# Performance work log

Hardware: AMD Instinct MI355X
Metric: run time of the kernel (lower is better)

## Reference

```python
import math
import jax, jax.numpy as jnp
import numpy as np

B, T, T_P, C, H = 4, 2048, 256, 768, 12
HD = C // H


def setup_inputs() -> dict:
    key = jax.random.key(0)
    k1, k2, k3, k4 = jax.random.split(key, 4)
    x = jax.random.normal(k1, (B, T, C), dtype=jnp.float32)
    prefix = jax.random.normal(k2, (B, T_P, C), dtype=jnp.float32)
    # torch nn.Linear weight layout: (out_features, in_features)
    W_qkv = jax.random.normal(k3, (3 * C, C), dtype=jnp.float32) * (1.0 / math.sqrt(C))
    W_out = jax.random.normal(k4, (C, C), dtype=jnp.float32) * (1.0 / math.sqrt(C))
    return {"x": x, "prefix": prefix, "W_qkv": W_qkv, "W_out": W_out}


def _mac_causal_mask(t_p: int, t: int) -> jnp.ndarray:
    total = t_p + t
    mask = jnp.zeros((total, total), dtype=bool)
    mask = mask.at[:t_p, t_p:].set(True)  # h tokens blocked from x tokens
    causal = jnp.triu(jnp.ones((t, t), dtype=bool), k=1)  # causal within x block
    return mask.at[t_p:, t_p:].set(causal)


def reference(x, prefix, W_qkv, W_out):
    b, t, c = x.shape
    t_p = prefix.shape[1]
    t_all = t_p + t
    x_full = jnp.concatenate([prefix, x], axis=1)          # (B, T_all, C)
    qkv = x_full @ W_qkv.T                                  # (B, T_all, 3C)
    q, k, v = jnp.split(qkv, 3, axis=-1)
    # (B, H, T_all, HD)
    q = q.reshape(b, t_all, H, HD).transpose(0, 2, 1, 3)
    k = k.reshape(b, t_all, H, HD).transpose(0, 2, 1, 3)
    v = v.reshape(b, t_all, H, HD).transpose(0, 2, 1, 3)
    scale = 1.0 / math.sqrt(HD)
    att = jnp.einsum('bhqd,bhkd->bhqk', q, k) * scale       # (B, H, T_all, T_all)
    mask = _mac_causal_mask(t_p, t)
    att = jnp.where(mask[None, None], -jnp.inf, att)
    att = jax.nn.softmax(att, axis=-1)                      # dropout = identity (eval)
    out = jnp.einsum('bhqk,bhkd->bhqd', att, v)             # (B, H, T_all, HD)
    out = out.transpose(0, 2, 1, 3).reshape(b, t_all, c)
    out = out @ W_out.T
    return out[:, t_p:, :]                                  # only x portion (B, T, C)
```

## Files before the change

### kernel.cpp

```cpp
#include <hip/hip_runtime.h>

constexpr int Bn   = 4;
constexpr int Tn   = 2048;
constexpr int TPn  = 256;
constexpr int TALLn = 2304;
constexpr int Cn   = 768;
constexpr int Hn   = 12;
constexpr int HDn  = 64;

typedef __bf16 bf16x4 __attribute__((ext_vector_type(4)));
typedef __bf16 bf16x8 __attribute__((ext_vector_type(8)));
typedef float  f32x4  __attribute__((ext_vector_type(4)));
typedef unsigned u32x4 __attribute__((ext_vector_type(4)));

__device__ __forceinline__ unsigned short f2bf(float f) {
    unsigned int x = __float_as_uint(f);
    x += 0x7fffu + ((x >> 16) & 1u);
    return (unsigned short)(x >> 16);
}

__device__ __forceinline__ unsigned cvt_pk_bf16(float a, float b) {
    unsigned r;
    asm("v_cvt_pk_bf16_f32 %0, %1, %2" : "=v"(r) : "v"(a), "v"(b));
    return r;
}

#define ASYNC16(gsrc, ldst)                                                           \
    __builtin_amdgcn_global_load_lds((__attribute__((address_space(1))) void*)(gsrc), \
                                     (__attribute__((address_space(3))) void*)(ldst), \
                                     16, 0, 0)

__global__ __launch_bounds__(256) void k_build_xfull(
        const float* __restrict__ x, const float* __restrict__ pre,
        unsigned short* __restrict__ xf) {
    int idx = blockIdx.x * 256 + threadIdx.x;
    int row = idx / (Cn / 4);
    int c   = (idx - row * (Cn / 4)) * 4;
    int b = row / TALLn, tt = row - b * TALLn;
    const float* src = (tt < TPn) ? pre + ((size_t)b * TPn + tt) * Cn + c
                                  : x   + ((size_t)b * Tn + (tt - TPn)) * Cn + c;
    float4 f = *reinterpret_cast<const float4*>(src);
    ushort4 o = { f2bf(f.x), f2bf(f.y), f2bf(f.z), f2bf(f.w) };
    *reinterpret_cast<ushort4*>(xf + (size_t)row * Cn + c) = o;
}

__global__ __launch_bounds__(256) void k_cast2(
        const float* __restrict__ wqkv, const float* __restrict__ wout,
        unsigned short* __restrict__ wqb, unsigned short* __restrict__ wob) {
    int idx = (blockIdx.x * 256 + threadIdx.x) * 4;
    const int n1 = 3 * Cn * Cn;
    const float* src;
    unsigned short* dst;
    if (idx < n1) { src = wqkv + idx; dst = wqb + idx; }
    else          { src = wout + (idx - n1); dst = wob + (idx - n1); }
    float4 f = *reinterpret_cast<const float4*>(src);
    ushort4 o = { f2bf(f.x), f2bf(f.y), f2bf(f.z), f2bf(f.w) };
    *reinterpret_cast<ushort4*>(dst) = o;
}

__global__ __launch_bounds__(256) void k_qkv_gemm(
        const unsigned short* __restrict__ A, const unsigned short* __restrict__ W,
        unsigned short* __restrict__ Qb, unsigned short* __restrict__ Kb,
        unsigned short* __restrict__ Vt) {
    __shared__ __align__(16) unsigned short smem[16384];
    const int tid  = threadIdx.x;
    const int wave = tid >> 6;
    const int lane = tid & 63;
    const int g = lane >> 4, l16 = lane & 15;
    const int m0 = blockIdx.x * 128, n0 = blockIdx.y * 128;
    const int wr = wave >> 1, wc = wave & 1;

    const unsigned short* pa[2];
    const unsigned short* pb[2];
    int sd[2];
    #pragma unroll
    for (int inst = 0; inst < 2; ++inst) {
        const int li = inst * 256 + tid;
        const int row = li >> 2;
        const int ch = (li & 3) ^ ((row >> 1) & 3);
        pa[inst] = A + (size_t)(m0 + row) * Cn + ch * 8;
        pb[inst] = W + (size_t)(n0 + row) * Cn + ch * 8;
        sd[inst] = (inst * 256 + wave * 64) * 8;
    }
    int aoff[4], boff[4];
    #pragma unroll
    for (int mt = 0; mt < 4; ++mt) {
        const int ra = wr * 64 + mt * 16 + l16;
        aoff[mt] = ra * 32 + ((g ^ ((ra >> 1) & 3)) << 3);
        const int rb = wc * 64 + mt * 16 + l16;
        boff[mt] = rb * 32 + ((g ^ ((rb >> 1) & 3)) << 3);
    }

    f32x4 acc[4][4] = {};

    #pragma unroll
    for (int inst = 0; inst < 2; ++inst) {
        ASYNC16(pa[inst], &smem[0]    + sd[inst]);
        ASYNC16(pb[inst], &smem[8192] + sd[inst]);
        pa[inst] += 32;
        pb[inst] += 32;
    }
    __syncthreads();

    int buf = 0;
    for (int kk = 0; kk < 24; ++kk) {
        if (kk + 1 < 24) {
            #pragma unroll
            for (int inst = 0; inst < 2; ++inst) {
                ASYNC16(pa[inst], &smem[(buf ^ 1) * 4096]        + sd[inst]);
                ASYNC16(pb[inst], &smem[8192 + (buf ^ 1) * 4096] + sd[inst]);
                pa[inst] += 32;
                pb[inst] += 32;
            }
        }
        const unsigned short* Ab = &smem[buf * 4096];
        const unsigned short* Bb = &smem[8192 + buf * 4096];
        bf16x8 af[4], bfv[4];
        #pragma unroll
        for (int mt = 0; mt < 4; ++mt) {
            af[mt]  = *reinterpret_cast<const bf16x8*>(&Ab[aoff[mt]]);
            bfv[mt] = *reinterpret_cast<const bf16x8*>(&Bb[boff[mt]]);
        }
        __builtin_amdgcn_s_setprio(1);
        #pragma unroll
        for (int mt = 0; mt < 4; ++mt)
            #pragma unroll
            for (int nt = 0; nt < 4; ++nt)
                acc[mt][nt] = __builtin_amdgcn_mfma_f32_16x16x32_bf16(
                        af[mt], bfv[nt], acc[mt][nt], 0, 0, 0);
        __builtin_amdgcn_s_setprio(0);
        buf ^= 1;
        __syncthreads();
    }

    const int b   = m0 / TALLn;
    const int t0  = m0 - b * TALLn;
    const int sel = n0 / Cn;
    const int hn0 = n0 - sel * Cn;
    constexpr float SCQ = 0.18033688011112042f;

    if (sel == 2) {
        #pragma unroll
        for (int mt = 0; mt < 4; ++mt)
            #pragma unroll
            for (int nt = 0; nt < 4; ++nt)
                #pragma unroll
                for (int r = 0; r < 4; ++r) {
                    const int t  = wr * 64 + mt * 16 + g * 4 + r;
                    const int hn = wc * 64 + nt * 16 + l16;
                    smem[hn * 128 + (((t >> 3) ^ (hn & 7)) << 3) + (t & 7)] =
                            f2bf(acc[mt][nt][r]);
                }
        __syncthreads();
        #pragma unroll
        for (int j = 0; j < 8; ++j) {
            const int u  = tid + 256 * j;
            const int hn = u >> 4, tc = u & 15;
            const int tile64 = tc >> 3;
            const int np = tc & 7;
            const int kg = np >> 2, gs = np & 3;
            const int tgA = tile64 * 8 + kg * 4 + (gs >> 1);
            const int sub = (gs & 1) * 4;
            bf16x4 rA = *reinterpret_cast<const bf16x4*>(
                    &smem[hn * 128 + ((tgA ^ (hn & 7)) << 3) + sub]);
            bf16x4 rB = *reinterpret_cast<const bf16x4*>(
                    &smem[hn * 128 + (((tgA + 2) ^ (hn & 7)) << 3) + sub]);
            bf16x8 v = __builtin_shufflevector(rA, rB, 0, 1, 2, 3, 4, 5, 6, 7);
            const int hh = (hn0 + hn) >> 6;
            const int dd = hn & 63;
            *reinterpret_cast<bf16x8*>(
                    &Vt[(((size_t)b * Hn + hh) * HDn + dd) * TALLn + t0 + tc * 8]) = v;
        }
    } else {
        #pragma unroll
        for (int mt = 0; mt < 4; ++mt)
            #pragma unroll
            for (int nt = 0; nt < 4; ++nt)
                #pragma unroll
                for (int r = 0; r < 4; ++r) {
                    const int t  = t0 + wr * 64 + mt * 16 + g * 4 + r;
                    const int hn = hn0 + wc * 64 + nt * 16 + l16;
                    const int h = hn >> 6, d = hn & 63;
                    if (sel == 0)
                        Qb[(((size_t)b * Hn + h) * TALLn + t) * HDn + d] =
                                f2bf(acc[mt][nt][r] * SCQ);
                    else
                        Kb[(((size_t)b * Hn + h) * TALLn + t) * HDn + d] =
                                f2bf(acc[mt][nt][r]);
                }
    }
}

__global__ __launch_bounds__(256) void k_attn(
        const unsigned short* __restrict__ Qb, const unsigned short* __restrict__ Kb,
        const unsigned short* __restrict__ Vt, unsigned short* __restrict__ Ob) {
    __shared__ __align__(16) unsigned short Ks[2][4096];
    __shared__ __align__(16) unsigned short Vs[2][4096];
    const int tid  = threadIdx.x;
    const int wq   = tid >> 6;
    const int lane = tid & 63;
    const int l16  = lane & 15;
    const int g    = lane >> 4;

    const int fb  = blockIdx.x;
    const int j   = fb >> 3;
    const int bh  = 6 * (fb & 7) + (j % 6);
    const int chunk = 31 - (j / 6);
    const int nkt = 5 + chunk;
    const size_t kv = (size_t)bh * TALLn * HDn;

    int koff[4][2];
    #pragma unroll
    for (int band = 0; band < 4; ++band)
        #pragma unroll
        for (int ks = 0; ks < 2; ++ks)
            koff[band][ks] = (band * 16 + l16) * 64 + (((ks * 4 + g) ^ (l16 & 7)) << 3);
    int voff[2];
    #pragma unroll
    for (int kg = 0; kg < 2; ++kg)
        voff[kg] = l16 * 64 + (((kg * 4 + g) ^ (l16 & 7)) << 3);
    const unsigned short* pk[2];
    const unsigned short* pv[2];
    int sdst[2];
    #pragma unroll
    for (int inst = 0; inst < 2; ++inst) {
        const int li = inst * 256 + tid;
        const int row = li >> 3;
        const int ch = (li & 7) ^ (row & 7);
        pk[inst] = Kb + kv + row * HDn + ch * 8;
        pv[inst] = Vt + kv + row * TALLn + ch * 8;
        sdst[inst] = (inst * 256 + wq * 64) * 8;
    }
    constexpr int KSTRIDE = 64 * HDn;
    constexpr int VSTRIDE = 64;

    bf16x8 qf[2];
    {
        const int tq = TPn + chunk * 64 + wq * 16 + l16;
        #pragma unroll
        for (int ks = 0; ks < 2; ++ks)
            qf[ks] = *reinterpret_cast<const bf16x8*>(
                    Qb + kv + (size_t)tq * HDn + ks * 32 + g * 8);
    }

    bf16x8 ones;
    #pragma unroll
    for (int i = 0; i < 8; ++i) ones[i] = (__bf16)1.0f;

    f32x4 oacc[4] = {};
    f32x4 lacc = {};

    #pragma unroll
    for (int inst = 0; inst < 2; ++inst) {
        ASYNC16(pk[inst], &Ks[0][0] + sdst[inst]);
        ASYNC16(pv[inst], &Vs[0][0] + sdst[inst]);
        pk[inst] += KSTRIDE;
        pv[inst] += VSTRIDE;
    }
    __syncthreads();

    int buf = 0;
    for (int t = 0; t < nkt; ++t) {
        if (t + 1 < nkt) {
            #pragma unroll
            for (int inst = 0; inst < 2; ++inst) {
                ASYNC16(pk[inst], &Ks[buf ^ 1][0] + sdst[inst]);
                ASYNC16(pv[inst], &Vs[buf ^ 1][0] + sdst[inst]);
                pk[inst] += KSTRIDE;
                pv[inst] += VSTRIDE;
            }
        }
        const unsigned short* Ksb = &Ks[buf][0];
        const unsigned short* Vsb = &Vs[buf][0];

        f32x4 sacc[4] = {};
        __builtin_amdgcn_s_setprio(1);
        #pragma unroll
        for (int band = 0; band < 4; ++band) {
            bf16x8 k0 = *reinterpret_cast<const bf16x8*>(&Ksb[koff[band][0]]);
            bf16x8 k1 = *reinterpret_cast<const bf16x8*>(&Ksb[koff[band][1]]);
            sacc[band] = __builtin_amdgcn_mfma_f32_16x16x32_bf16(
                    k0, qf[0], sacc[band], 0, 0, 0);
            sacc[band] = __builtin_amdgcn_mfma_f32_16x16x32_bf16(
                    k1, qf[1], sacc[band], 0, 0, 0);
        }
        __builtin_amdgcn_s_setprio(0);

        if (t == nkt - 1) {
            const int lim = TPn + chunk * 64 + wq * 16 + l16 - t * 64;
            #pragma unroll
            for (int band = 0; band < 4; ++band)
                #pragma unroll
                for (int r = 0; r < 4; ++r)
                    sacc[band][r] = (band * 16 + g * 4 + r <= lim) ? sacc[band][r]
                                                                   : -1e30f;
        }
        unsigned dwb[4][2];
        #pragma unroll
        for (int band = 0; band < 4; ++band) {
            const float e0 = exp2f(sacc[band][0]);
            const float e1 = exp2f(sacc[band][1]);
            const float e2 = exp2f(sacc[band][2]);
            const float e3 = exp2f(sacc[band][3]);
            dwb[band][0] = cvt_pk_bf16(e0, e1);
            dwb[band][1] = cvt_pk_bf16(e2, e3);
        }

        __builtin_amdgcn_s_setprio(1);
        #pragma unroll
        for (int kg = 0; kg < 2; ++kg) {
            const u32x4 uu = { dwb[2 * kg][0], dwb[2 * kg][1],
                               dwb[2 * kg + 1][0], dwb[2 * kg + 1][1] };
            const bf16x8 pf = __builtin_bit_cast(bf16x8, uu);
            lacc = __builtin_amdgcn_mfma_f32_16x16x32_bf16(ones, pf, lacc, 0, 0, 0);
            #pragma unroll
            for (int dband = 0; dband < 4; ++dband) {
                bf16x8 vf = *reinterpret_cast<const bf16x8*>(
                        &Vsb[dband * 1024 + voff[kg]]);
                oacc[dband] = __builtin_amdgcn_mfma_f32_16x16x32_bf16(
                        vf, pf, oacc[dband], 0, 0, 0);
            }
        }
        __builtin_amdgcn_s_setprio(0);

        buf ^= 1;
        __syncthreads();
    }

    const int b = bh / Hn, h = bh - b * Hn;
    const float inv = 1.0f / lacc[0];
    const size_t row = (size_t)b * Tn + chunk * 64 + wq * 16 + l16;
    #pragma unroll
    for (int dband = 0; dband < 4; ++dband) {
        ushort4 st;
        st.x = f2bf(oacc[dband][0] * inv);
        st.y = f2bf(oacc[dband][1] * inv);
        st.z = f2bf(oacc[dband][2] * inv);
        st.w = f2bf(oacc[dband][3] * inv);
        *reinterpret_cast<ushort4*>(&Ob[row * Cn + h * 64 + dband * 16 + g * 4]) = st;
    }
}

__global__ __launch_bounds__(256) void k_out_gemm(
        const unsigned short* __restrict__ A, const unsigned short* __restrict__ W,
        float* __restrict__ out) {
    __shared__ __align__(16) unsigned short smem[16384];
    const int tid  = threadIdx.x;
    const int wave = tid >> 6;
    const int lane = tid & 63;
    const int g = lane >> 4, l16 = lane & 15;
    const int m0 = blockIdx.x * 128, n0 = blockIdx.y * 128;
    const int wr = wave >> 1, wc = wave & 1;

    const unsigned short* pa[2];
    const unsigned short* pb[2];
    int sd[2];
    #pragma unroll
    for (int inst = 0; inst < 2; ++inst) {
        const int li = inst * 256 + tid;
        const int row = li >> 2;
        const int ch = (li & 3) ^ ((row >> 1) & 3);
        pa[inst] = A + (size_t)(m0 + row) * Cn + ch * 8;
        pb[inst] = W + (size_t)(n0 + row) * Cn + ch * 8;
        sd[inst] = (inst * 256 + wave * 64) * 8;
    }
    int aoff[4], boff[4];
    #pragma unroll
    for (int mt = 0; mt < 4; ++mt) {
        const int ra = wr * 64 + mt * 16 + l16;
        aoff[mt] = ra * 32 + ((g ^ ((ra >> 1) & 3)) << 3);
        const int rb = wc * 64 + mt * 16 + l16;
        boff[mt] = rb * 32 + ((g ^ ((rb >> 1) & 3)) << 3);
    }

    f32x4 acc[4][4] = {};

    #pragma unroll
    for (int inst = 0; inst < 2; ++inst) {
        ASYNC16(pa[inst], &smem[0]    + sd[inst]);
        ASYNC16(pb[inst], &smem[8192] + sd[inst]);
        pa[inst] += 32;
        pb[inst] += 32;
    }
    __syncthreads();

    int buf = 0;
    for (int kk = 0; kk < 24; ++kk) {
        if (kk + 1 < 24) {
            #pragma unroll
            for (int inst = 0; inst < 2; ++inst) {
                ASYNC16(pa[inst], &smem[(buf ^ 1) * 4096]        + sd[inst]);
                ASYNC16(pb[inst], &smem[8192 + (buf ^ 1) * 4096] + sd[inst]);
                pa[inst] += 32;
                pb[inst] += 32;
            }
        }
        const unsigned short* Ab = &smem[buf * 4096];
        const unsigned short* Bb = &smem[8192 + buf * 4096];
        bf16x8 af[4], bfv[4];
        #pragma unroll
        for (int mt = 0; mt < 4; ++mt) {
            af[mt]  = *reinterpret_cast<const bf16x8*>(&Ab[aoff[mt]]);
            bfv[mt] = *reinterpret_cast<const bf16x8*>(&Bb[boff[mt]]);
        }
        __builtin_amdgcn_s_setprio(1);
        #pragma unroll
        for (int mt = 0; mt < 4; ++mt)
            #pragma unroll
            for (int nt = 0; nt < 4; ++nt)
                acc[mt][nt] = __builtin_amdgcn_mfma_f32_16x16x32_bf16(
                        af[mt], bfv[nt], acc[mt][nt], 0, 0, 0);
        __builtin_amdgcn_s_setprio(0);
        buf ^= 1;
        __syncthreads();
    }

    #pragma unroll
    for (int mt = 0; mt < 4; ++mt)
        #pragma unroll
        for (int nt = 0; nt < 4; ++nt)
            #pragma unroll
            for (int r = 0; r < 4; ++r) {
                const int m = m0 + wr * 64 + mt * 16 + g * 4 + r;
                const int n = n0 + wc * 64 + nt * 16 + l16;
                out[(size_t)m * Cn + n] = acc[mt][nt][r];
            }
}

extern "C" void kernel_launch(void* const* d_in, const int* in_sizes, int n_in,
                              void* d_out, int out_size, void* d_ws, size_t ws_size,
                              hipStream_t stream) {
    const float* x    = (const float*)d_in[0];
    const float* pre  = (const float*)d_in[1];
    const float* wqkv = (const float*)d_in[2];
    const float* wout = (const float*)d_in[3];
    float* out = (float*)d_out;
    char* ws = (char*)d_ws;

    unsigned short* xf  = (unsigned short*)(ws + 0);
    unsigned short* wqb = (unsigned short*)(ws + 14155776);
    unsigned short* wob = (unsigned short*)(ws + 17694720);
    unsigned short* Qb  = (unsigned short*)(ws + 18874368);
    unsigned short* Kb  = (unsigned short*)(ws + 33030144);
    unsigned short* Vt  = (unsigned short*)(ws + 47185920);
    unsigned short* Ob  = (unsigned short*)(ws + 61341696);

    k_build_xfull<<<dim3((Bn * TALLn * Cn / 4) / 256), 256, 0, stream>>>(x, pre, xf);
    k_cast2<<<dim3((4 * Cn * Cn / 4) / 256), 256, 0, stream>>>(wqkv, wout, wqb, wob);
    k_qkv_gemm<<<dim3((Bn * TALLn) / 128, (3 * Cn) / 128), 256, 0, stream>>>(
            xf, wqb, Qb, Kb, Vt);
    k_attn<<<dim3(1536), 256, 0, stream>>>(Qb, Kb, Vt, Ob);
    k_out_gemm<<<dim3((Bn * Tn) / 128, Cn / 128), 256, 0, stream>>>(Ob, wob, out);
}
```

Before: 141.2 us.

## Merge prep casts into one kernel and shrink output GEMM tile to 64x128

Merges the x_full build and the weight-cast kernels into a single launch, saving one kernel launch and its tail. The output projection GEMM changes from 128x128 to 64x128 tiles with each wave owning a 64x32 slice, doubling the block count. This gives more blocks across the CUs for the 8192x768 output, at the cost of less reuse per tile. It also simplifies the causal mask limit on the diagonal tile, which should hold if the last key tile always aligns with the query chunk.

```diff
diff --git a/kernel.cpp b/kernel.cpp
--- a/kernel.cpp
+++ b/kernel.cpp
@@ -30,29 +30,28 @@
                                      (__attribute__((address_space(3))) void*)(ldst), \
                                      16, 0, 0)
 
-__global__ __launch_bounds__(256) void k_build_xfull(
+__global__ __launch_bounds__(256) void k_prep(
         const float* __restrict__ x, const float* __restrict__ pre,
-        unsigned short* __restrict__ xf) {
-    int idx = blockIdx.x * 256 + threadIdx.x;
-    int row = idx / (Cn / 4);
-    int c   = (idx - row * (Cn / 4)) * 4;
-    int b = row / TALLn, tt = row - b * TALLn;
-    const float* src = (tt < TPn) ? pre + ((size_t)b * TPn + tt) * Cn + c
-                                  : x   + ((size_t)b * Tn + (tt - TPn)) * Cn + c;
-    float4 f = *reinterpret_cast<const float4*>(src);
-    ushort4 o = { f2bf(f.x), f2bf(f.y), f2bf(f.z), f2bf(f.w) };
-    *reinterpret_cast<ushort4*>(xf + (size_t)row * Cn + c) = o;
-}
-
-__global__ __launch_bounds__(256) void k_cast2(
         const float* __restrict__ wqkv, const float* __restrict__ wout,
-        unsigned short* __restrict__ wqb, unsigned short* __restrict__ wob) {
-    int idx = (blockIdx.x * 256 + threadIdx.x) * 4;
-    const int n1 = 3 * Cn * Cn;
+        unsigned short* __restrict__ xf, unsigned short* __restrict__ wqb,
+        unsigned short* __restrict__ wob) {
+    const int idx = blockIdx.x * 256 + threadIdx.x;
+    constexpr int NXF = Bn * TALLn * Cn / 4;
+    constexpr int NW1 = 3 * Cn * Cn / 4;
     const float* src;
     unsigned short* dst;
-    if (idx < n1) { src = wqkv + idx; dst = wqb + idx; }
-    else          { src = wout + (idx - n1); dst = wob + (idx - n1); }
+    if (idx < NXF) {
+        const int row = idx / (Cn / 4);
+        const int c   = (idx - row * (Cn / 4)) * 4;
+        const int b = row / TALLn, tt = row - b * TALLn;
+        src = (tt < TPn) ? pre + ((size_t)b * TPn + tt) * Cn + c
+                         : x   + ((size_t)b * Tn + (tt - TPn)) * Cn + c;
+        dst = xf + (size_t)row * Cn + c;
+    } else {
+        const int k = idx - NXF;
+        if (k < NW1) { src = wqkv + (size_t)k * 4; dst = wqb + (size_t)k * 4; }
+        else { src = wout + (size_t)(k - NW1) * 4; dst = wob + (size_t)(k - NW1) * 4; }
+    }
     float4 f = *reinterpret_cast<const float4*>(src);
     ushort4 o = { f2bf(f.x), f2bf(f.y), f2bf(f.z), f2bf(f.w) };
     *reinterpret_cast<ushort4*>(dst) = o;
@@ -287,7 +286,7 @@
         __builtin_amdgcn_s_setprio(0);
 
         if (t == nkt - 1) {
-            const int lim = TPn + chunk * 64 + wq * 16 + l16 - t * 64;
+            const int lim = wq * 16 + l16;
             #pragma unroll
             for (int band = 0; band < 4; ++band)
                 #pragma unroll
@@ -344,42 +343,50 @@
 __global__ __launch_bounds__(256) void k_out_gemm(
         const unsigned short* __restrict__ A, const unsigned short* __restrict__ W,
         float* __restrict__ out) {
-    __shared__ __align__(16) unsigned short smem[16384];
+    __shared__ __align__(16) unsigned short As[2][2048];
+    __shared__ __align__(16) unsigned short Bs[2][4096];
     const int tid  = threadIdx.x;
-    const int wave = tid >> 6;
+    const int wq   = tid >> 6;
     const int lane = tid & 63;
     const int g = lane >> 4, l16 = lane & 15;
-    const int m0 = blockIdx.x * 128, n0 = blockIdx.y * 128;
-    const int wr = wave >> 1, wc = wave & 1;
-
-    const unsigned short* pa[2];
+    const int m0 = blockIdx.x * 64, n0 = blockIdx.y * 128;
+
+    const unsigned short* pa;
     const unsigned short* pb[2];
-    int sd[2];
+    int sdA, sdB[2];
+    {
+        const int row = tid >> 2;
+        const int ch = (tid & 3) ^ ((row >> 1) & 3);
+        pa = A + (size_t)(m0 + row) * Cn + ch * 8;
+        sdA = wq * 512;
+    }
     #pragma unroll
     for (int inst = 0; inst < 2; ++inst) {
         const int li = inst * 256 + tid;
         const int row = li >> 2;
         const int ch = (li & 3) ^ ((row >> 1) & 3);
-        pa[inst] = A + (size_t)(m0 + row) * Cn + ch * 8;
         pb[inst] = W + (size_t)(n0 + row) * Cn + ch * 8;
-        sd[inst] = (inst * 256 + wave * 64) * 8;
-    }
-    int aoff[4], boff[4];
+        sdB[inst] = (inst * 256 + wq * 64) * 8;
+    }
+    int aoff[4], boff[2];
     #pragma unroll
     for (int mt = 0; mt < 4; ++mt) {
-        const int ra = wr * 64 + mt * 16 + l16;
+        const int ra = mt * 16 + l16;
         aoff[mt] = ra * 32 + ((g ^ ((ra >> 1) & 3)) << 3);
-        const int rb = wc * 64 + mt * 16 + l16;
-        boff[mt] = rb * 32 + ((g ^ ((rb >> 1) & 3)) << 3);
-    }
-
-    f32x4 acc[4][4] = {};
-
-    #pragma unroll
-    for (int inst = 0; inst < 2; ++inst) {
-        ASYNC16(pa[inst], &smem[0]    + sd[inst]);
-        ASYNC16(pb[inst], &smem[8192] + sd[inst]);
-        pa[inst] += 32;
+    }
+    #pragma unroll
+    for (int nt = 0; nt < 2; ++nt) {
+        const int rb = wq * 32 + nt * 16 + l16;
+        boff[nt] = rb * 32 + ((g ^ ((rb >> 1) & 3)) << 3);
+    }
+
+    f32x4 acc[4][2] = {};
+
+    ASYNC16(pa, &As[0][0] + sdA);
+    pa += 32;
+    #pragma unroll
+    for (int inst = 0; inst < 2; ++inst) {
+        ASYNC16(pb[inst], &Bs[0][0] + sdB[inst]);
         pb[inst] += 32;
     }
     __syncthreads();
@@ -387,27 +394,26 @@
     int buf = 0;
     for (int kk = 0; kk < 24; ++kk) {
         if (kk + 1 < 24) {
+            ASYNC16(pa, &As[buf ^ 1][0] + sdA);
+            pa += 32;
             #pragma unroll
             for (int inst = 0; inst < 2; ++inst) {
-                ASYNC16(pa[inst], &smem[(buf ^ 1) * 4096]        + sd[inst]);
-                ASYNC16(pb[inst], &smem[8192 + (buf ^ 1) * 4096] + sd[inst]);
-                pa[inst] += 32;
+                ASYNC16(pb[inst], &Bs[buf ^ 1][0] + sdB[inst]);
                 pb[inst] += 32;
             }
         }
-        const unsigned short* Ab = &smem[buf * 4096];
-        const unsigned short* Bb = &smem[8192 + buf * 4096];
-        bf16x8 af[4], bfv[4];
-        #pragma unroll
-        for (int mt = 0; mt < 4; ++mt) {
-            af[mt]  = *reinterpret_cast<const bf16x8*>(&Ab[aoff[mt]]);
-            bfv[mt] = *reinterpret_cast<const bf16x8*>(&Bb[boff[mt]]);
-        }
+        bf16x8 af[4], bfv[2];
+        #pragma unroll
+        for (int mt = 0; mt < 4; ++mt)
+            af[mt] = *reinterpret_cast<const bf16x8*>(&As[buf][aoff[mt]]);
+        #pragma unroll
+        for (int nt = 0; nt < 2; ++nt)
+            bfv[nt] = *reinterpret_cast<const bf16x8*>(&Bs[buf][boff[nt]]);
         __builtin_amdgcn_s_setprio(1);
         #pragma unroll
         for (int mt = 0; mt < 4; ++mt)
             #pragma unroll
-            for (int nt = 0; nt < 4; ++nt)
+            for (int nt = 0; nt < 2; ++nt)
                 acc[mt][nt] = __builtin_amdgcn_mfma_f32_16x16x32_bf16(
                         af[mt], bfv[nt], acc[mt][nt], 0, 0, 0);
         __builtin_amdgcn_s_setprio(0);
@@ -418,11 +424,11 @@
     #pragma unroll
     for (int mt = 0; mt < 4; ++mt)
         #pragma unroll
-        for (int nt = 0; nt < 4; ++nt)
+        for (int nt = 0; nt < 2; ++nt)
             #pragma unroll
             for (int r = 0; r < 4; ++r) {
-                const int m = m0 + wr * 64 + mt * 16 + g * 4 + r;
-                const int n = n0 + wc * 64 + nt * 16 + l16;
+                const int m = m0 + mt * 16 + g * 4 + r;
+                const int n = n0 + wq * 32 + nt * 16 + l16;
                 out[(size_t)m * Cn + n] = acc[mt][nt][r];
             }
 }
@@ -445,10 +451,10 @@
     unsigned short* Vt  = (unsigned short*)(ws + 47185920);
     unsigned short* Ob  = (unsigned short*)(ws + 61341696);
 
-    k_build_xfull<<<dim3((Bn * TALLn * Cn / 4) / 256), 256, 0, stream>>>(x, pre, xf);
-    k_cast2<<<dim3((4 * Cn * Cn / 4) / 256), 256, 0, stream>>>(wqkv, wout, wqb, wob);
+    constexpr int PREP_UNITS = (Bn * TALLn * Cn + 4 * Cn * Cn) / 4;
+    k_prep<<<dim3(PREP_UNITS / 256), 256, 0, stream>>>(x, pre, wqkv, wout, xf, wqb, wob);
     k_qkv_gemm<<<dim3((Bn * TALLn) / 128, (3 * Cn) / 128), 256, 0, stream>>>(
             xf, wqb, Qb, Kb, Vt);
     k_attn<<<dim3(1536), 256, 0, stream>>>(Qb, Kb, Vt, Ob);
-    k_out_gemm<<<dim3((Bn * Tn) / 128, Cn / 128), 256, 0, stream>>>(Ob, wob, out);
-}
+    k_out_gemm<<<dim3((Bn * Tn) / 64, Cn / 128), 256, 0, stream>>>(Ob, wob, out);
+}
```

Result: no change. 142.9 us (+1.2%).
